# Performance work log

Hardware: AMD Instinct MI355X
Metric: run time of the kernel (lower is better)

Reference implementation:

```python
import jax, jax.numpy as jnp
import numpy as np

DT = 0.042
B, L, N_INP, N_HID = 128, 512, 96, 1024


def setup_inputs() -> dict:
    key = jax.random.key(0)
    k_x, k_x2h, k_h2h, k_b, k_g, k_e = jax.random.split(key, 6)
    x = jax.random.normal(k_x, (B, L, N_INP), dtype=jnp.float32)
    # x2h = rand(n_inp, n_hid) * input_scaling (input_scaling = 1.0)
    x2h = jax.random.uniform(k_x2h, (N_INP, N_HID), dtype=jnp.float32)
    # h2h = 2*(2*rand-1) then spectral-norm scaled to rho=0.99; emulate scale statistics
    h2h = 2.0 * (2.0 * jax.random.uniform(k_h2h, (N_HID, N_HID), dtype=jnp.float32) - 1.0)
    # approximate spectral normalization: scale by rho / ||h2h||_2 (power-iteration-free proxy via norm)
    sv = jnp.linalg.norm(h2h, ord=2)
    h2h = h2h * (0.99 / sv)
    bias = (2.0 * jax.random.uniform(k_b, (N_HID,), dtype=jnp.float32) - 1.0)
    # gamma ~ U[2.7, 4.7], epsilon ~ U[4.7, 6.7] per-unit vectors
    gamma = jax.random.uniform(k_g, (N_HID,), dtype=jnp.float32) * 2.0 + 2.7
    epsilon = jax.random.uniform(k_e, (N_HID,), dtype=jnp.float32) * 2.0 + 4.7
    return {"x": x, "x2h": x2h, "h2h": h2h, "bias": bias, "gamma": gamma, "epsilon": epsilon}


def reference(x, x2h, h2h, bias, gamma, epsilon):
    # Precompute input projection for all timesteps: (B, L, H)
    xw = jnp.einsum('bli,ih->blh', x, x2h) + bias
    hy0 = jnp.zeros((x.shape[0], h2h.shape[0]), dtype=x.dtype)
    hz0 = jnp.zeros_like(hy0)

    def step(carry, xt):  # xt: (B, H)
        hy, hz = carry
        hz = hz + DT * (jnp.tanh(xt + hy @ h2h) - gamma * hy - epsilon * hz)
        hy = hy + DT * hz
        return (hy, hz), hy

    (hy, hz), ys = jax.lax.scan(step, (hy0, hz0), jnp.swapaxes(xw, 0, 1))
    all_states = jnp.swapaxes(ys, 0, 1)  # (B, L, H)
    return all_states
```

## Files before the change

kernel.cpp:

```cpp
#include <hip/hip_runtime.h>
#include <math.h>

typedef short short8 __attribute__((ext_vector_type(8)));
typedef float f32x4 __attribute__((ext_vector_type(4)));
typedef unsigned long long u64;
typedef u64 u64x2 __attribute__((ext_vector_type(2)));

#define DT 0.042f
#define LSEQ 512
#define NI 96
#define NH 1024

static __device__ __forceinline__ unsigned short f2bf(float f) {
  unsigned int u = __builtin_bit_cast(unsigned int, f);
  return (unsigned short)((u + 0x7fffu + ((u >> 16) & 1u)) >> 16);
}
static __device__ __forceinline__ float bf2f(unsigned short h) {
  unsigned int u = ((unsigned int)h) << 16;
  return __builtin_bit_cast(float, u);
}
static __device__ __forceinline__ float fast_tanhf(float a) {
  float ax = __builtin_fabsf(a);
  float e = __expf(2.0f * ax);
  float t = 1.0f - 2.0f / (e + 1.0f);
  return a < 0.0f ? -t : t;
}

__global__ __launch_bounds__(512, 2) void ron_kernel(
    const float* __restrict__ x, const float* __restrict__ x2h,
    const float* __restrict__ h2h, const float* __restrict__ bias,
    const float* __restrict__ gam_, const float* __restrict__ eps_,
    float* __restrict__ out, unsigned int* __restrict__ flags,
    unsigned int* __restrict__ hy_ex) {
  const int tid = threadIdx.x;
  const int w = tid >> 6;
  const int l = tid & 63;
  const int g = blockIdx.x & 7;
  const int jb = blockIdx.x >> 3;
  const int lc = l & 15;
  const int kg = l >> 4;

  __shared__ f32x4 part[8][2][64];

  short8 wfh[4][2], wfl[4][2];
#pragma unroll
  for (int j = 0; j < 4; ++j) {
    const int krow = (w * 4 + j) * 32 + kg * 8;
#pragma unroll
    for (int t = 0; t < 2; ++t) {
      const int c = jb * 32 + t * 16 + lc;
#pragma unroll
      for (int jj = 0; jj < 8; ++jj) {
        float v = h2h[(size_t)(krow + jj) * NH + c];
        unsigned short hb = f2bf(v);
        wfh[j][t][jj] = (short)hb;
        wfl[j][t][jj] = (short)f2bf(v - bf2f(hb));
      }
    }
  }
  const int myc = jb * 32 + w * 16 + lc;
  short8 xwh[3], xwl[3];
  float bias_c = 0.f, gam = 0.f, ep = 0.f;
  if (w < 2) {
#pragma unroll
    for (int kt = 0; kt < 3; ++kt)
#pragma unroll
      for (int jj = 0; jj < 8; ++jj) {
        float v = x2h[(size_t)(kt * 32 + kg * 8 + jj) * NH + myc];
        unsigned short hb = f2bf(v);
        xwh[kt][jj] = (short)hb;
        xwl[kt][jj] = (short)f2bf(v - bf2f(hb));
      }
    bias_c = bias[myc];
    gam = gam_[myc];
    ep = eps_[myc];
  }

  float hy[4] = {0.f, 0.f, 0.f, 0.f};
  float hz[4] = {0.f, 0.f, 0.f, 0.f};
  const float* xlane = x + (size_t)(g * 16 + lc) * LSEQ * NI + kg * 8;
  const int aoff = lc * 8 + kg * 2;
  unsigned int* myflag = flags + (size_t)(g * 32 + jb) * 16;
  unsigned int* watch = flags + (size_t)(g * 32 + w * 4 + (l & 3)) * 16;
  const int ktc = myc >> 5, kgc = (myc >> 3) & 3, sh = myc & 7;

  f32x4 xr[6];
  if (w < 2) {
    const float* xs = xlane;
#pragma unroll
    for (int kt = 0; kt < 3; ++kt) {
      xr[2 * kt] = *(const f32x4*)(xs + kt * 32);
      xr[2 * kt + 1] = *(const f32x4*)(xs + kt * 32 + 4);
    }
  }

  for (int s = 0; s < LSEQ; ++s) {
    const int wb = s % 3;
    const int rb = wb ? wb - 1 : 2;

    short8 axh[3], axl[3];
    if (w < 2) {
#pragma unroll
      for (int kt = 0; kt < 3; ++kt) {
#pragma unroll
        for (int jj = 0; jj < 4; ++jj) {
          unsigned short hb = f2bf(xr[2 * kt][jj]);
          axh[kt][jj] = (short)hb;
          axl[kt][jj] = (short)f2bf(xr[2 * kt][jj] - bf2f(hb));
          unsigned short hb2 = f2bf(xr[2 * kt + 1][jj]);
          axh[kt][jj + 4] = (short)hb2;
          axl[kt][jj + 4] = (short)f2bf(xr[2 * kt + 1][jj] - bf2f(hb2));
        }
      }
      const float* xs2 = xlane + (size_t)(s + 1 < LSEQ ? s + 1 : s) * NI;
#pragma unroll
      for (int kt = 0; kt < 3; ++kt) {
        xr[2 * kt] = *(const f32x4*)(xs2 + kt * 32);
        xr[2 * kt + 1] = *(const f32x4*)(xs2 + kt * 32 + 4);
      }
    }

    f32x4 a0a = {0.f, 0.f, 0.f, 0.f}, a0b = {0.f, 0.f, 0.f, 0.f};
    f32x4 a1a = {0.f, 0.f, 0.f, 0.f}, a1b = {0.f, 0.f, 0.f, 0.f};
    f32x4 accx = {0.f, 0.f, 0.f, 0.f};
    u64 ah0[4], ah1[4], al0[4], al1[4];

    if (s) {
      int guard = 0;
      for (;;) {
        unsigned int v = __hip_atomic_load(watch, __ATOMIC_RELAXED, __HIP_MEMORY_SCOPE_AGENT);
        if (!__any((int)v < s)) break;
        if (++guard > (1 << 18)) break;
        __builtin_amdgcn_s_sleep(1);
      }
      asm volatile("" ::: "memory");

      const u64* srcg = (const u64*)hy_ex + (size_t)(rb * 8 + g) * 8192;
#pragma unroll
      for (int j = 0; j < 4; ++j) {
        const int idx = (w * 4 + j) * 128 + aoff;
        ah0[j] = __hip_atomic_load(srcg + idx, __ATOMIC_RELAXED, __HIP_MEMORY_SCOPE_AGENT);
        ah1[j] = __hip_atomic_load(srcg + idx + 1, __ATOMIC_RELAXED, __HIP_MEMORY_SCOPE_AGENT);
        al0[j] = __hip_atomic_load(srcg + 4096 + idx, __ATOMIC_RELAXED, __HIP_MEMORY_SCOPE_AGENT);
        al1[j] = __hip_atomic_load(srcg + 4096 + idx + 1, __ATOMIC_RELAXED, __HIP_MEMORY_SCOPE_AGENT);
      }
    }

    if (w < 2) {
#pragma unroll
      for (int kt = 0; kt < 3; ++kt) {
        accx = __builtin_amdgcn_mfma_f32_16x16x32_bf16(axh[kt], xwh[kt], accx, 0, 0, 0);
        accx = __builtin_amdgcn_mfma_f32_16x16x32_bf16(axl[kt], xwh[kt], accx, 0, 0, 0);
        accx = __builtin_amdgcn_mfma_f32_16x16x32_bf16(axh[kt], xwl[kt], accx, 0, 0, 0);
      }
    }

    if (s) {
#pragma unroll
      for (int j = 0; j < 4; ++j) {
        short8 fh = __builtin_bit_cast(short8, (u64x2){ah0[j], ah1[j]});
        short8 fl = __builtin_bit_cast(short8, (u64x2){al0[j], al1[j]});
        if (j & 1) {
          a0b = __builtin_amdgcn_mfma_f32_16x16x32_bf16(fh, wfh[j][0], a0b, 0, 0, 0);
          a1b = __builtin_amdgcn_mfma_f32_16x16x32_bf16(fh, wfh[j][1], a1b, 0, 0, 0);
          a0b = __builtin_amdgcn_mfma_f32_16x16x32_bf16(fl, wfh[j][0], a0b, 0, 0, 0);
          a1b = __builtin_amdgcn_mfma_f32_16x16x32_bf16(fl, wfh[j][1], a1b, 0, 0, 0);
          a0b = __builtin_amdgcn_mfma_f32_16x16x32_bf16(fh, wfl[j][0], a0b, 0, 0, 0);
          a1b = __builtin_amdgcn_mfma_f32_16x16x32_bf16(fh, wfl[j][1], a1b, 0, 0, 0);
        } else {
          a0a = __builtin_amdgcn_mfma_f32_16x16x32_bf16(fh, wfh[j][0], a0a, 0, 0, 0);
          a1a = __builtin_amdgcn_mfma_f32_16x16x32_bf16(fh, wfh[j][1], a1a, 0, 0, 0);
          a0a = __builtin_amdgcn_mfma_f32_16x16x32_bf16(fl, wfh[j][0], a0a, 0, 0, 0);
          a1a = __builtin_amdgcn_mfma_f32_16x16x32_bf16(fl, wfh[j][1], a1a, 0, 0, 0);
          a0a = __builtin_amdgcn_mfma_f32_16x16x32_bf16(fh, wfl[j][0], a0a, 0, 0, 0);
          a1a = __builtin_amdgcn_mfma_f32_16x16x32_bf16(fh, wfl[j][1], a1a, 0, 0, 0);
        }
      }
    }

    part[w][0][l] = a0a + a0b;
    part[w][1][l] = a1a + a1b;
    __syncthreads();

    if (w < 2) {
      f32x4 r = accx;
#pragma unroll
      for (int ww = 0; ww < 8; ++ww) r += part[ww][w][l];

      unsigned int* dstg = hy_ex + (size_t)(wb * 8 + g) * 16384;
#pragma unroll
      for (int i = 0; i < 4; ++i) {
        float a = r[i] + bias_c;
        float th = fast_tanhf(a);
        hz[i] += DT * (th - gam * hy[i] - ep * hz[i]);
        hy[i] += DT * hz[i];
        const int rr = kg * 4 + i;
        unsigned short hb = f2bf(hy[i]);
        unsigned short lb = f2bf(hy[i] - bf2f(hb));
        unsigned int oh = (unsigned int)__shfl_xor((int)hb, 1, 64);
        unsigned int ol = (unsigned int)__shfl_xor((int)lb, 1, 64);
        if (!(lc & 1)) {
          const int u32idx = (ktc * 512 + rr * 32 + kgc * 8 + sh) >> 1;
          __hip_atomic_store(dstg + u32idx, (unsigned int)hb | (oh << 16),
                             __ATOMIC_RELAXED, __HIP_MEMORY_SCOPE_AGENT);
          __hip_atomic_store(dstg + 8192 + u32idx, (unsigned int)lb | (ol << 16),
                             __ATOMIC_RELAXED, __HIP_MEMORY_SCOPE_AGENT);
        }
      }
    }

    asm volatile("" ::: "memory");
    __syncthreads();
    if (tid == 0)
      __hip_atomic_store(myflag, (unsigned int)(s + 1), __ATOMIC_RELAXED,
                         __HIP_MEMORY_SCOPE_AGENT);

    if (w < 2) {
#pragma unroll
      for (int i = 0; i < 4; ++i)
        out[((size_t)(g * 16 + kg * 4 + i) * LSEQ + s) * NH + myc] = hy[i];
    }
  }
}

extern "C" void kernel_launch(void* const* d_in, const int* in_sizes, int n_in,
                              void* d_out, int out_size, void* d_ws, size_t ws_size,
                              hipStream_t stream) {
  const float* x = (const float*)d_in[0];
  const float* x2h = (const float*)d_in[1];
  const float* h2h = (const float*)d_in[2];
  const float* bias = (const float*)d_in[3];
  const float* gam = (const float*)d_in[4];
  const float* eps = (const float*)d_in[5];
  float* out = (float*)d_out;

  unsigned int* flags = (unsigned int*)d_ws;
  unsigned int* hy_ex = (unsigned int*)((char*)d_ws + 16384);

  hipMemsetAsync(d_ws, 0, 16384, stream);

  ron_kernel<<<dim3(256), dim3(512), 0, stream>>>(x, x2h, h2h, bias, gam, eps, out, flags, hy_ex);
}
```

Baseline: 1.874 ms.

## Remap workgroups so each batch group shares one XCD and use XCD-local exchange loads

After: 1.798 ms, median of 2. 4.1% less time.

```diff
diff --git a/kernel.cpp b/kernel.cpp
--- a/kernel.cpp
+++ b/kernel.cpp
@@ -25,6 +25,36 @@
   float t = 1.0f - 2.0f / (e + 1.0f);
   return a < 0.0f ? -t : t;
 }
+
+template <bool F>
+static __device__ __forceinline__ void ld16_issue(u64x2* dst, const u64* p) {
+  if constexpr (F) {
+    asm volatile("global_load_dwordx4 %0, %1, off sc0" : "=v"(*dst) : "v"(p) : "memory");
+  } else {
+    u64 a = __hip_atomic_load(p, __ATOMIC_RELAXED, __HIP_MEMORY_SCOPE_AGENT);
+    u64 b = __hip_atomic_load(p + 1, __ATOMIC_RELAXED, __HIP_MEMORY_SCOPE_AGENT);
+    *dst = (u64x2){a, b};
+  }
+}
+template <bool F>
+static __device__ __forceinline__ void ld_fence() {
+  if constexpr (F) {
+    asm volatile("s_waitcnt vmcnt(0)" ::: "memory");
+    __builtin_amdgcn_sched_barrier(0);
+  }
+}
+template <bool F>
+static __device__ __forceinline__ void stpub(unsigned int* p, unsigned int v) {
+  if constexpr (F)
+    asm volatile("global_store_dword %0, %1, off sc0" ::"v"(p), "v"(v) : "memory");
+  else
+    __hip_atomic_store(p, v, __ATOMIC_RELAXED, __HIP_MEMORY_SCOPE_AGENT);
+}
+static __device__ __forceinline__ void drain_vm() {
+  asm volatile("s_waitcnt vmcnt(0)" ::: "memory");
+  __builtin_amdgcn_sched_barrier(0);
+}
+template <bool B> struct BoolC { static constexpr bool value = B; };
 
 __global__ __launch_bounds__(512, 2) void ron_kernel(
     const float* __restrict__ x, const float* __restrict__ x2h,
@@ -35,12 +65,91 @@
   const int tid = threadIdx.x;
   const int w = tid >> 6;
   const int l = tid & 63;
-  const int g = blockIdx.x & 7;
-  const int jb = blockIdx.x >> 3;
   const int lc = l & 15;
   const int kg = l >> 4;
 
   __shared__ f32x4 part[8][2][64];
+  __shared__ int info_sh;
+
+  unsigned int* base = flags + 4096;
+  unsigned int* xcdtab = base;
+  unsigned int* ctr = base + 256;
+  unsigned int* abortw = base + 257;
+  unsigned int* enttab = base + 272;
+
+  if (tid == 0) {
+    unsigned int myxcd = __builtin_amdgcn_s_getreg(63508) & 15u;
+    __hip_atomic_store(xcdtab + blockIdx.x, 0x100u | myxcd, __ATOMIC_RELAXED,
+                       __HIP_MEMORY_SCOPE_AGENT);
+    __hip_atomic_fetch_add(ctr, 1u, __ATOMIC_RELAXED, __HIP_MEMORY_SCOPE_AGENT);
+  }
+
+  if (blockIdx.x == 0 && tid == 0) {
+    int gu = 0;
+    while (__hip_atomic_load(ctr, __ATOMIC_RELAXED, __HIP_MEMORY_SCOPE_AGENT) < 256u) {
+      if (++gu > (1 << 17)) break;
+      __builtin_amdgcn_s_sleep(8);
+    }
+    bool ok = (gu <= (1 << 17));
+    unsigned char xs[256];
+    if (ok) {
+      for (int i = 0; i < 256; ++i) {
+        unsigned int v = __hip_atomic_load(xcdtab + i, __ATOMIC_RELAXED, __HIP_MEMORY_SCOPE_AGENT);
+        int g2 = 0;
+        while (v == 0 && ++g2 <= 8192) {
+          __builtin_amdgcn_s_sleep(2);
+          v = __hip_atomic_load(xcdtab + i, __ATOMIC_RELAXED, __HIP_MEMORY_SCOPE_AGENT);
+        }
+        if (v == 0) { ok = false; break; }
+        xs[i] = (unsigned char)(v & 15u);
+      }
+    }
+    unsigned int ent[256];
+    if (ok) {
+      int gidx = 0, nl = 0;
+      unsigned char left[256], tmp[256];
+      for (unsigned int xc = 0; xc < 16u && gidx < 8; ++xc) {
+        int cnt = 0;
+        for (int i = 0; i < 256; ++i)
+          if (xs[i] == (unsigned char)xc) tmp[cnt++] = (unsigned char)i;
+        int p = 0;
+        while (cnt - p >= 32 && gidx < 8) {
+          for (int k2 = 0; k2 < 32; ++k2)
+            ent[tmp[p + k2]] = 1u | ((unsigned)gidx << 1) | ((unsigned)k2 << 4) | (1u << 9);
+          ++gidx; p += 32;
+        }
+        for (; p < cnt; ++p) left[nl++] = tmp[p];
+      }
+      int li = 0;
+      while (gidx < 8) {
+        for (int k2 = 0; k2 < 32 && li < nl; ++k2, ++li)
+          ent[left[li]] = 1u | ((unsigned)gidx << 1) | ((unsigned)k2 << 4);
+        ++gidx;
+      }
+    } else {
+      for (int i = 0; i < 256; ++i)
+        ent[i] = 1u | ((unsigned)(i & 7) << 1) | ((unsigned)(i >> 3) << 4);
+    }
+    for (int i = 0; i < 256; ++i)
+      __hip_atomic_store(enttab + i, ent[i], __ATOMIC_RELAXED, __HIP_MEMORY_SCOPE_AGENT);
+  }
+
+  if (tid == 0) {
+    unsigned int e = 0;
+    int gu = 0;
+    for (;;) {
+      e = __hip_atomic_load(enttab + blockIdx.x, __ATOMIC_RELAXED, __HIP_MEMORY_SCOPE_AGENT);
+      if (e || ++gu > (1 << 17)) break;
+      __builtin_amdgcn_s_sleep(16);
+    }
+    if (!e) e = 1u | ((unsigned)(blockIdx.x & 7) << 1) | ((unsigned)(blockIdx.x >> 3) << 4);
+    info_sh = (int)e;
+  }
+  __syncthreads();
+  const unsigned int ent = (unsigned int)info_sh;
+  const int g = (ent >> 1) & 7;
+  const int jb = (ent >> 4) & 31;
+  const bool fastm = ((ent >> 9) & 1) != 0;
 
   short8 wfh[4][2], wfl[4][2];
 #pragma unroll
@@ -86,141 +195,155 @@
 
   f32x4 xr[6];
   if (w < 2) {
-    const float* xs = xlane;
 #pragma unroll
     for (int kt = 0; kt < 3; ++kt) {
-      xr[2 * kt] = *(const f32x4*)(xs + kt * 32);
-      xr[2 * kt + 1] = *(const f32x4*)(xs + kt * 32 + 4);
-    }
-  }
-
-  for (int s = 0; s < LSEQ; ++s) {
-    const int wb = s % 3;
-    const int rb = wb ? wb - 1 : 2;
-
-    short8 axh[3], axl[3];
-    if (w < 2) {
-#pragma unroll
-      for (int kt = 0; kt < 3; ++kt) {
-#pragma unroll
-        for (int jj = 0; jj < 4; ++jj) {
-          unsigned short hb = f2bf(xr[2 * kt][jj]);
-          axh[kt][jj] = (short)hb;
-          axl[kt][jj] = (short)f2bf(xr[2 * kt][jj] - bf2f(hb));
-          unsigned short hb2 = f2bf(xr[2 * kt + 1][jj]);
-          axh[kt][jj + 4] = (short)hb2;
-          axl[kt][jj + 4] = (short)f2bf(xr[2 * kt + 1][jj] - bf2f(hb2));
-        }
-      }
-      const float* xs2 = xlane + (size_t)(s + 1 < LSEQ ? s + 1 : s) * NI;
-#pragma unroll
-      for (int kt = 0; kt < 3; ++kt) {
-        xr[2 * kt] = *(const f32x4*)(xs2 + kt * 32);
-        xr[2 * kt + 1] = *(const f32x4*)(xs2 + kt * 32 + 4);
-      }
-    }
-
-    f32x4 a0a = {0.f, 0.f, 0.f, 0.f}, a0b = {0.f, 0.f, 0.f, 0.f};
-    f32x4 a1a = {0.f, 0.f, 0.f, 0.f}, a1b = {0.f, 0.f, 0.f, 0.f};
-    f32x4 accx = {0.f, 0.f, 0.f, 0.f};
-    u64 ah0[4], ah1[4], al0[4], al1[4];
-
-    if (s) {
-      int guard = 0;
-      for (;;) {
-        unsigned int v = __hip_atomic_load(watch, __ATOMIC_RELAXED, __HIP_MEMORY_SCOPE_AGENT);
-        if (!__any((int)v < s)) break;
-        if (++guard > (1 << 18)) break;
-        __builtin_amdgcn_s_sleep(1);
-      }
-      asm volatile("" ::: "memory");
-
-      const u64* srcg = (const u64*)hy_ex + (size_t)(rb * 8 + g) * 8192;
-#pragma unroll
-      for (int j = 0; j < 4; ++j) {
-        const int idx = (w * 4 + j) * 128 + aoff;
-        ah0[j] = __hip_atomic_load(srcg + idx, __ATOMIC_RELAXED, __HIP_MEMORY_SCOPE_AGENT);
-        ah1[j] = __hip_atomic_load(srcg + idx + 1, __ATOMIC_RELAXED, __HIP_MEMORY_SCOPE_AGENT);
-        al0[j] = __hip_atomic_load(srcg + 4096 + idx, __ATOMIC_RELAXED, __HIP_MEMORY_SCOPE_AGENT);
-        al1[j] = __hip_atomic_load(srcg + 4096 + idx + 1, __ATOMIC_RELAXED, __HIP_MEMORY_SCOPE_AGENT);
-      }
-    }
-
-    if (w < 2) {
-#pragma unroll
-      for (int kt = 0; kt < 3; ++kt) {
-        accx = __builtin_amdgcn_mfma_f32_16x16x32_bf16(axh[kt], xwh[kt], accx, 0, 0, 0);
-        accx = __builtin_amdgcn_mfma_f32_16x16x32_bf16(axl[kt], xwh[kt], accx, 0, 0, 0);
-        accx = __builtin_amdgcn_mfma_f32_16x16x32_bf16(axh[kt], xwl[kt], accx, 0, 0, 0);
-      }
-    }
-
-    if (s) {
-#pragma unroll
-      for (int j = 0; j < 4; ++j) {
-        short8 fh = __builtin_bit_cast(short8, (u64x2){ah0[j], ah1[j]});
-        short8 fl = __builtin_bit_cast(short8, (u64x2){al0[j], al1[j]});
-        if (j & 1) {
-          a0b = __builtin_amdgcn_mfma_f32_16x16x32_bf16(fh, wfh[j][0], a0b, 0, 0, 0);
-          a1b = __builtin_amdgcn_mfma_f32_16x16x32_bf16(fh, wfh[j][1], a1b, 0, 0, 0);
-          a0b = __builtin_amdgcn_mfma_f32_16x16x32_bf16(fl, wfh[j][0], a0b, 0, 0, 0);
-          a1b = __builtin_amdgcn_mfma_f32_16x16x32_bf16(fl, wfh[j][1], a1b, 0, 0, 0);
-          a0b = __builtin_amdgcn_mfma_f32_16x16x32_bf16(fh, wfl[j][0], a0b, 0, 0, 0);
-          a1b = __builtin_amdgcn_mfma_f32_16x16x32_bf16(fh, wfl[j][1], a1b, 0, 0, 0);
-        } else {
-          a0a = __builtin_amdgcn_mfma_f32_16x16x32_bf16(fh, wfh[j][0], a0a, 0, 0, 0);
-          a1a = __builtin_amdgcn_mfma_f32_16x16x32_bf16(fh, wfh[j][1], a1a, 0, 0, 0);
-          a0a = __builtin_amdgcn_mfma_f32_16x16x32_bf16(fl, wfh[j][0], a0a, 0, 0, 0);
-          a1a = __builtin_amdgcn_mfma_f32_16x16x32_bf16(fl, wfh[j][1], a1a, 0, 0, 0);
-          a0a = __builtin_amdgcn_mfma_f32_16x16x32_bf16(fh, wfl[j][0], a0a, 0, 0, 0);
-          a1a = __builtin_amdgcn_mfma_f32_16x16x32_bf16(fh, wfl[j][1], a1a, 0, 0, 0);
-        }
-      }
-    }
-
-    part[w][0][l] = a0a + a0b;
-    part[w][1][l] = a1a + a1b;
-    __syncthreads();
-
-    if (w < 2) {
-      f32x4 r = accx;
-#pragma unroll
-      for (int ww = 0; ww < 8; ++ww) r += part[ww][w][l];
-
-      unsigned int* dstg = hy_ex + (size_t)(wb * 8 + g) * 16384;
-#pragma unroll
-      for (int i = 0; i < 4; ++i) {
-        float a = r[i] + bias_c;
-        float th = fast_tanhf(a);
-        hz[i] += DT * (th - gam * hy[i] - ep * hz[i]);
-        hy[i] += DT * hz[i];
-        const int rr = kg * 4 + i;
-        unsigned short hb = f2bf(hy[i]);
-        unsigned short lb = f2bf(hy[i] - bf2f(hb));
-        unsigned int oh = (unsigned int)__shfl_xor((int)hb, 1, 64);
-        unsigned int ol = (unsigned int)__shfl_xor((int)lb, 1, 64);
-        if (!(lc & 1)) {
-          const int u32idx = (ktc * 512 + rr * 32 + kgc * 8 + sh) >> 1;
-          __hip_atomic_store(dstg + u32idx, (unsigned int)hb | (oh << 16),
-                             __ATOMIC_RELAXED, __HIP_MEMORY_SCOPE_AGENT);
-          __hip_atomic_store(dstg + 8192 + u32idx, (unsigned int)lb | (ol << 16),
-                             __ATOMIC_RELAXED, __HIP_MEMORY_SCOPE_AGENT);
-        }
-      }
-    }
-
-    asm volatile("" ::: "memory");
-    __syncthreads();
-    if (tid == 0)
-      __hip_atomic_store(myflag, (unsigned int)(s + 1), __ATOMIC_RELAXED,
-                         __HIP_MEMORY_SCOPE_AGENT);
-
-    if (w < 2) {
-#pragma unroll
-      for (int i = 0; i < 4; ++i)
-        out[((size_t)(g * 16 + kg * 4 + i) * LSEQ + s) * NH + myc] = hy[i];
-    }
-  }
+      xr[2 * kt] = *(const f32x4*)(xlane + kt * 32);
+      xr[2 * kt + 1] = *(const f32x4*)(xlane + kt * 32 + 4);
+    }
+  }
+
+  auto run = [&](auto fc) {
+    constexpr bool F = decltype(fc)::value;
+    bool noSync = false;
+    for (int s = 0; s < LSEQ; ++s) {
+      const int wb = s % 3;
+      const int rb = wb ? wb - 1 : 2;
+
+      short8 axh[3], axl[3];
+      if (w < 2) {
+#pragma unroll
+        for (int kt = 0; kt < 3; ++kt) {
+#pragma unroll
+          for (int jj = 0; jj < 4; ++jj) {
+            unsigned short hb = f2bf(xr[2 * kt][jj]);
+            axh[kt][jj] = (short)hb;
+            axl[kt][jj] = (short)f2bf(xr[2 * kt][jj] - bf2f(hb));
+            unsigned short hb2 = f2bf(xr[2 * kt + 1][jj]);
+            axh[kt][jj + 4] = (short)hb2;
+            axl[kt][jj + 4] = (short)f2bf(xr[2 * kt + 1][jj] - bf2f(hb2));
+          }
+        }
+      }
+
+      f32x4 a0a = {0.f, 0.f, 0.f, 0.f}, a0b = {0.f, 0.f, 0.f, 0.f};
+      f32x4 a1a = {0.f, 0.f, 0.f, 0.f}, a1b = {0.f, 0.f, 0.f, 0.f};
+      f32x4 accx = {0.f, 0.f, 0.f, 0.f};
+      u64x2 hq[4], lq[4];
+
+      if (s) {
+        if (!noSync) {
+          int guard = 0;
+          for (;;) {
+            unsigned int v = __hip_atomic_load(watch, __ATOMIC_RELAXED, __HIP_MEMORY_SCOPE_AGENT);
+            if (!__any((int)v < s)) break;
+            if ((++guard & 255) == 0) {
+              if (__hip_atomic_load(abortw, __ATOMIC_RELAXED, __HIP_MEMORY_SCOPE_AGENT) != 0u ||
+                  guard > (1 << 16)) {
+                __hip_atomic_store(abortw, 1u, __ATOMIC_RELAXED, __HIP_MEMORY_SCOPE_AGENT);
+                noSync = true;
+                break;
+              }
+            }
+            __builtin_amdgcn_s_sleep(1);
+          }
+        }
+        asm volatile("" ::: "memory");
+
+        const u64* srcg = (const u64*)hy_ex + (size_t)(rb * 8 + g) * 8192;
+#pragma unroll
+        for (int j = 0; j < 4; ++j) {
+          const int idx = (w * 4 + j) * 128 + aoff;
+          ld16_issue<F>(&hq[j], srcg + idx);
+          ld16_issue<F>(&lq[j], srcg + 4096 + idx);
+        }
+      }
+
+      if (w < 2) {
+#pragma unroll
+        for (int kt = 0; kt < 3; ++kt) {
+          accx = __builtin_amdgcn_mfma_f32_16x16x32_bf16(axh[kt], xwh[kt], accx, 0, 0, 0);
+          accx = __builtin_amdgcn_mfma_f32_16x16x32_bf16(axl[kt], xwh[kt], accx, 0, 0, 0);
+          accx = __builtin_amdgcn_mfma_f32_16x16x32_bf16(axh[kt], xwl[kt], accx, 0, 0, 0);
+        }
+      }
+
+      if (s) {
+        ld_fence<F>();
+#pragma unroll
+        for (int j = 0; j < 4; ++j) {
+          short8 fh = __builtin_bit_cast(short8, hq[j]);
+          short8 fl = __builtin_bit_cast(short8, lq[j]);
+          if (j & 1) {
+            a0b = __builtin_amdgcn_mfma_f32_16x16x32_bf16(fh, wfh[j][0], a0b, 0, 0, 0);
+            a1b = __builtin_amdgcn_mfma_f32_16x16x32_bf16(fh, wfh[j][1], a1b, 0, 0, 0);
+            a0b = __builtin_amdgcn_mfma_f32_16x16x32_bf16(fl, wfh[j][0], a0b, 0, 0, 0);
+            a1b = __builtin_amdgcn_mfma_f32_16x16x32_bf16(fl, wfh[j][1], a1b, 0, 0, 0);
+            a0b = __builtin_amdgcn_mfma_f32_16x16x32_bf16(fh, wfl[j][0], a0b, 0, 0, 0);
+            a1b = __builtin_amdgcn_mfma_f32_16x16x32_bf16(fh, wfl[j][1], a1b, 0, 0, 0);
+          } else {
+            a0a = __builtin_amdgcn_mfma_f32_16x16x32_bf16(fh, wfh[j][0], a0a, 0, 0, 0);
+            a1a = __builtin_amdgcn_mfma_f32_16x16x32_bf16(fh, wfh[j][1], a1a, 0, 0, 0);
+            a0a = __builtin_amdgcn_mfma_f32_16x16x32_bf16(fl, wfh[j][0], a0a, 0, 0, 0);
+            a1a = __builtin_amdgcn_mfma_f32_16x16x32_bf16(fl, wfh[j][1], a1a, 0, 0, 0);
+            a0a = __builtin_amdgcn_mfma_f32_16x16x32_bf16(fh, wfl[j][0], a0a, 0, 0, 0);
+            a1a = __builtin_amdgcn_mfma_f32_16x16x32_bf16(fh, wfl[j][1], a1a, 0, 0, 0);
+          }
+        }
+      }
+
+      part[w][0][l] = a0a + a0b;
+      part[w][1][l] = a1a + a1b;
+      __syncthreads();
+
+      if (w < 2) {
+        f32x4 r = accx;
+#pragma unroll
+        for (int ww = 0; ww < 8; ++ww) r += part[ww][w][l];
+
+        unsigned int* dstg = hy_ex + (size_t)(wb * 8 + g) * 16384;
+#pragma unroll
+        for (int i = 0; i < 4; ++i) {
+          float a = r[i] + bias_c;
+          float th = fast_tanhf(a);
+          hz[i] += DT * (th - gam * hy[i] - ep * hz[i]);
+          hy[i] += DT * hz[i];
+          const int rr = kg * 4 + i;
+          unsigned short hb = f2bf(hy[i]);
+          unsigned short lb = f2bf(hy[i] - bf2f(hb));
+          unsigned int oh = (unsigned int)__shfl_xor((int)hb, 1, 64);
+          unsigned int ol = (unsigned int)__shfl_xor((int)lb, 1, 64);
+          if (!(lc & 1)) {
+            const int u32idx = (ktc * 512 + rr * 32 + kgc * 8 + sh) >> 1;
+            stpub<F>(dstg + u32idx, (unsigned int)hb | (oh << 16));
+            stpub<F>(dstg + 8192 + u32idx, (unsigned int)lb | (ol << 16));
+          }
+        }
+      }
+
+      drain_vm();
+      __syncthreads();
+      if (tid == 0)
+        __hip_atomic_store(myflag, (unsigned int)(s + 1), __ATOMIC_RELAXED,
+                           __HIP_MEMORY_SCOPE_AGENT);
+
+      if (w < 2) {
+#pragma unroll
+        for (int i = 0; i < 4; ++i)
+          out[((size_t)(g * 16 + kg * 4 + i) * LSEQ + s) * NH + myc] = hy[i];
+        const float* xs2 = xlane + (size_t)(s + 1 < LSEQ ? s + 1 : s) * NI;
+#pragma unroll
+        for (int kt = 0; kt < 3; ++kt) {
+          xr[2 * kt] = *(const f32x4*)(xs2 + kt * 32);
+          xr[2 * kt + 1] = *(const f32x4*)(xs2 + kt * 32 + 4);
+        }
+      }
+    }
+  };
+
+  if (fastm)
+    run(BoolC<true>{});
+  else
+    run(BoolC<false>{});
 }
 
 extern "C" void kernel_launch(void* const* d_in, const int* in_sizes, int n_in,
@@ -235,9 +358,9 @@
   float* out = (float*)d_out;
 
   unsigned int* flags = (unsigned int*)d_ws;
-  unsigned int* hy_ex = (unsigned int*)((char*)d_ws + 16384);
-
-  hipMemsetAsync(d_ws, 0, 16384, stream);
+  unsigned int* hy_ex = (unsigned int*)((char*)d_ws + 32768);
+
+  hipMemsetAsync(d_ws, 0, 32768, stream);
 
   ron_kernel<<<dim3(256), dim3(512), 0, stream>>>(x, x2h, h2h, bias, gam, eps, out, flags, hy_ex);
 }
```
